# Kernel tuning notes

Measured on AMD Instinct MI355X. Metric: run time of the kernel, lower is better.

Reference implementation:

```python
import jax, jax.numpy as jnp
import numpy as np

XLIM = 10.0
N_BINS = 200
LATTICE = 12.42
N_O, N_H = 64, 128
T, R = 1000, 8


def setup_inputs() -> dict:
    key = jax.random.key(0)
    k1, k2 = jax.random.split(key)
    n = N_O + N_H
    stacked_radii = jax.random.uniform(k1, (T, R, n, 3), dtype=jnp.float32) * LATTICE
    lattices = jnp.full((3,), LATTICE, dtype=jnp.float32)
    gt_rdf = jax.random.uniform(k2, (3, N_BINS), dtype=jnp.float32)
    idx_O = jnp.arange(N_O, dtype=jnp.int32)
    idx_H = jnp.arange(N_H, dtype=jnp.int32) + N_O
    return {"stacked_radii": stacked_radii, "lattices": lattices,
            "gt_rdf": gt_rdf, "idx_O": idx_O, "idx_H": idx_H}


def reference(stacked_radii, lattices, gt_rdf, idx_O, idx_H):
    bins = jnp.linspace(1e-6, XLIM, N_BINS + 1, dtype=jnp.float32)
    # np.histogram normalization: rho * (4/3)pi (r_hi^3 - r_lo^3)
    shell = (4.0 / 3.0) * np.pi * (bins[1:] ** 3 - bins[:-1] ** 3)
    vol = jnp.prod(lattices)
    # wrap positions into the box (data_seq / L % 1 * L)
    x = stacked_radii / lattices % 1.0 * lattices
    x = jnp.transpose(x, (1, 0, 2, 3))  # [R, T, N, 3]

    def pair_rdf(x_rep, i0, i1):
        x0 = x_rep[:, i0]  # [T, n0, 3]
        x1 = x_rep[:, i1]  # [T, n1, 3]
        # all-pairs minimum-image distance under PBC
        delta = jnp.abs(x0[:, :, None, :] - x1[:, None, :, :])  # [T, n0, n1, 3]
        delta = jnp.where(delta > 0.5 * lattices, delta - lattices, delta)
        d = jnp.sqrt(jnp.sum(delta ** 2, axis=-1)).ravel()
        n_pairs = d.shape[0]  # includes zeros, matches original rho
        mask = (d != 0.0) & (d >= bins[0]) & (d <= bins[-1])
        bidx = jnp.clip(jnp.searchsorted(bins, d, side='right') - 1, 0, N_BINS - 1)
        hist = jax.ops.segment_sum(mask.astype(jnp.float32), bidx, num_segments=N_BINS)
        rho = n_pairs / vol
        return hist / (rho * shell)  # [N_BINS]

    pairs = [(idx_O, idx_O), (idx_H, idx_H), (idx_H, idx_O)]  # OO, HH, HO
    # sequential over replicas (like the original python loop) to bound memory
    rdfs = [jax.lax.map(lambda xr, i0=i0, i1=i1: pair_rdf(xr, i0, i1), x)
            for (i0, i1) in pairs]  # each [R, N_BINS]
    maes = jnp.stack([XLIM * jnp.mean(jnp.abs(r - g), axis=-1)
                      for r, g in zip(rdfs, gt_rdf)], axis=0)  # [3, R]
    max_maes = jnp.max(maes, axis=0)  # [R]
    rdf_stack = jnp.concatenate(rdfs, axis=-1)  # [R, 3*N_BINS]
    return rdf_stack, max_maes
```

## Files before the change

kernel.cpp:

```cpp
#include <hip/hip_runtime.h>
#include <math.h>

#define NUM_T   1000
#define NUM_R   8
#define NBINS   200
#define FPB     4
#define NCOPY   8
#define HSTR    601
#define TTSZ    224

__device__ __forceinline__ float approx_sqrt(float x) {
    float r; asm("v_sqrt_f32 %0, %1" : "=v"(r) : "v"(x)); return r;
}
__device__ __forceinline__ float fract_(float x) {
#if __has_builtin(__builtin_amdgcn_fractf)
    return __builtin_amdgcn_fractf(x);
#else
    return x - floorf(x);
#endif
}

__global__ __launch_bounds__(256) void rdf_hist_kernel(
    const float* __restrict__ radii,
    const float* __restrict__ lat,
    unsigned int* __restrict__ gh)
{
    #pragma clang fp contract(off)
    __shared__ float4 posOx[96], posH0[96], posH1[96];
    __shared__ float TT[TTSZ];
    __shared__ unsigned int hist[NCOPY * HSTR];

    const int tid = threadIdx.x;

    if (tid < TTSZ) {
        float v;
        if (tid <= 200) {
            float b;
            if (tid < NBINS) {
                const double step = (10.0 - 1e-6) / 200.0;
                b = (float)(1e-6 + (double)tid * step);
            } else {
                b = __uint_as_float(__float_as_uint(10.0f) + 1u);
            }
            unsigned lo = 0u, hi = 0x7F800000u;
            while (lo < hi) {
                unsigned mid = (lo + hi) >> 1;
                if (sqrtf(__uint_as_float(mid)) >= b) hi = mid; else lo = mid + 1;
            }
            v = __uint_as_float(lo);
        } else {
            v = __uint_as_float(0x7F800000u);
        }
        TT[tid] = v;
    }
    for (int i = tid; i < NCOPY * HSTR; i += 256) hist[i] = 0u;

    const float Lx = lat[0], Ly = lat[1], Lz = lat[2];
    __syncthreads();

    const float Tp = TT[200];
    const int   hc = ((tid >> 3) & (NCOPY - 1)) * HSTR;

#define PAIR(PI, PJ, HB, W)                                                  \
    {                                                                        \
        float tx = (PI).x - (PJ).x;                                          \
        float ty = (PI).y - (PJ).y;                                          \
        float tz = (PI).z - (PJ).z;                                          \
        float ax = fminf(fabsf(tx), Lx - fabsf(tx));                         \
        float ay = fminf(fabsf(ty), Ly - fabsf(ty));                         \
        float az = fminf(fabsf(tz), Lz - fabsf(tz));                         \
        float s  = (ax*ax + ay*ay) + az*az;                                  \
        float z  = approx_sqrt(s * 400.0f);                                  \
        int   k  = (int)z;                                                   \
        float m  = fract_(z);                                                \
        if (__builtin_expect(fabsf(m - 0.5f) > 0.49980f, 0)) {               \
            float tlo = TT[k], thi = TT[k + 1];                              \
            k += ((s >= thi) ? 1 : 0) - ((s < tlo) ? 1 : 0);                 \
            k = max(k, 0);                                                   \
        }                                                                    \
        if (s < Tp) atomicAdd(&hist[(HB) + k], (W));                         \
    }

    const int rep   = blockIdx.x & (NUM_R - 1);
    const int chunk = blockIdx.x / NUM_R;
    const int iO = tid & 63;
    const int q  = tid >> 6;
    const int hO = tid & 127;
    const int qh = tid >> 7;

    for (int f = 0; f < FPB; ++f) {
        const int t = chunk * FPB + f;
        const float* src = radii + ((size_t)t * NUM_R + rep) * (192 * 3);
        __syncthreads();
        if (tid < 192) {
            float vx = src[tid*3+0], vy = src[tid*3+1], vz = src[tid*3+2];
            float ux = vx / Lx; ux -= floorf(ux);
            float uy = vy / Ly; uy -= floorf(uy);
            float uz = vz / Lz; uz -= floorf(uz);
            float4 p = make_float4(ux*Lx, uy*Ly, uz*Lz, 0.0f);
            if (tid < 64)       { posOx[tid] = p;        if (tid < 32)  posOx[tid+64] = p; }
            else if (tid < 128) { int h = tid-64;  posH0[h] = p; if (h < 32) posH0[h+64] = p; }
            else                { int h = tid-128; posH1[h] = p; if (h < 32) posH1[h+64] = p; }
        }
        __syncthreads();

        {
            const float4 pi = posOx[iO];
            const int hb = hc + 0 * NBINS;
            const int jb = iO + q + 1;
            #pragma unroll
            for (int it = 0; it < 7; ++it) { float4 pj = posOx[jb + 4*it]; PAIR(pi, pj, hb, 2u); }
            if (q < 3 || iO < 32)          { float4 pj = posOx[jb + 28];   PAIR(pi, pj, hb, 2u); }
        }
        {
            const float4 pi = posH0[iO];
            const int hb = hc + 1 * NBINS;
            const int jb = iO + q + 1;
            #pragma unroll
            for (int it = 0; it < 7; ++it) { float4 pj = posH0[jb + 4*it]; PAIR(pi, pj, hb, 2u); }
            if (q < 3 || iO < 32)          { float4 pj = posH0[jb + 28];   PAIR(pi, pj, hb, 2u); }
        }
        {
            const float4 pi = posH1[iO];
            const int hb = hc + 1 * NBINS;
            const int jb = iO + q + 1;
            #pragma unroll
            for (int it = 0; it < 7; ++it) { float4 pj = posH1[jb + 4*it]; PAIR(pi, pj, hb, 2u); }
            if (q < 3 || iO < 32)          { float4 pj = posH1[jb + 28];   PAIR(pi, pj, hb, 2u); }
        }
        {
            const float4 pi = posH0[iO];
            const int hb = hc + 1 * NBINS;
            const int jb = q * 16;
            #pragma unroll
            for (int jj = 0; jj < 16; ++jj) { float4 pj = posH1[jb + jj]; PAIR(pi, pj, hb, 2u); }
        }
        {
            const float4 pi = (hO < 64) ? posH0[hO] : posH1[hO - 64];
            const int hb = hc + 2 * NBINS;
            const int jb = qh * 32;
            #pragma unroll
            for (int jj = 0; jj < 32; ++jj) { float4 pj = posOx[jb + jj]; PAIR(pi, pj, hb, 1u); }
        }
    }
#undef PAIR

    __syncthreads();
    for (int i = tid; i < 3 * NBINS; i += 256) {
        unsigned int v = 0;
        #pragma unroll
        for (int c = 0; c < NCOPY; ++c) v += hist[c * HSTR + i];
        if (v) atomicAdd(&gh[rep * 3 * NBINS + i], v);
    }
}

__global__ __launch_bounds__(256) void rdf_final_kernel(
    const unsigned int* __restrict__ gh,
    const float* __restrict__ gt,
    const float* __restrict__ lat,
    float* __restrict__ out)
{
    #pragma clang fp contract(off)
    const int rep = blockIdx.x;
    const int tid = threadIdx.x;
    __shared__ float bins[NBINS + 1];
    __shared__ float red[256];

    for (int i = tid; i <= NBINS; i += 256) {
        const double step = (10.0 - 1e-6) / 200.0;
        bins[i] = (i == NBINS) ? 10.0f : (float)(1e-6 + (double)i * step);
    }
    __syncthreads();

    const float vol = (lat[0] * lat[1]) * lat[2];
    const float C   = 4.18879020478639053f;
    const int npairs[3] = { NUM_T*64*64, NUM_T*128*128, NUM_T*128*64 };

    float maxmae = -3.0e38f;
    for (int p = 0; p < 3; ++p) {
        float diff = 0.0f;
        if (tid < NBINS) {
            float b0 = bins[tid], b1 = bins[tid + 1];
            float shell = C * (b1*b1*b1 - b0*b0*b0);
            float rho = (float)npairs[p] / vol;
            float g = (float)gh[(rep*3 + p)*NBINS + tid] / (rho * shell);
            out[rep*3*NBINS + p*NBINS + tid] = g;
            diff = fabsf(g - gt[p*NBINS + tid]);
        }
        red[tid] = diff;
        __syncthreads();
        for (int s = 128; s > 0; s >>= 1) {
            if (tid < s) red[tid] += red[tid + s];
            __syncthreads();
        }
        if (tid == 0) {
            float mae = 10.0f * (red[0] / 200.0f);
            if (mae > maxmae) maxmae = mae;
        }
        __syncthreads();
    }
    if (tid == 0) out[NUM_R*3*NBINS + rep] = maxmae;
}

extern "C" void kernel_launch(void* const* d_in, const int* in_sizes, int n_in,
                              void* d_out, int out_size, void* d_ws, size_t ws_size,
                              hipStream_t stream) {
    const float* radii = (const float*)d_in[0];
    const float* lat   = (const float*)d_in[1];
    const float* gt    = (const float*)d_in[2];
    unsigned int* gh   = (unsigned int*)d_ws;

    hipMemsetAsync(gh, 0, NUM_R * 3 * NBINS * sizeof(unsigned int), stream);

    dim3 grid(NUM_R * (NUM_T / FPB));
    hipLaunchKernelGGL(rdf_hist_kernel, grid, dim3(256), 0, stream,
                       radii, lat, gh);
    hipLaunchKernelGGL(rdf_final_kernel, dim3(NUM_R), dim3(256), 0, stream,
                       gh, gt, lat, (float*)d_out);
}
```

Measured before the change: 109.7 us.

## Prefetch next frame, branchless out-of-range atomics, wave-uniform ambiguity check, halve frames per block

Loads the next frame's raw positions into registers while the current frame's pairs are processed, so global latency overlaps compute. Replaces the per-lane range test with an unsigned-bit range compare that sends out-of-range pairs to a dummy bin (600) instead of predicating the atomic. It also makes the bin-boundary fixup branch wave-uniform via __any, and restructures the HO loop so each thread handles both H sets against shared O positions. FPB drops from 4 to 2, doubling the number of blocks. The cost is more LDS atomics on the dummy bin, which may contend, plus extra fixed setup per block.

Result: faster. 106.7 us (-2.7%).

```diff
diff --git a/kernel.cpp b/kernel.cpp
--- a/kernel.cpp
+++ b/kernel.cpp
@@ -4,7 +4,7 @@
 #define NUM_T   1000
 #define NUM_R   8
 #define NBINS   200
-#define FPB     4
+#define FPB     2
 #define NCOPY   8
 #define HSTR    601
 #define TTSZ    224
@@ -58,10 +58,11 @@
     const float Lx = lat[0], Ly = lat[1], Lz = lat[2];
     __syncthreads();
 
-    const float Tp = TT[200];
-    const int   hc = ((tid >> 3) & (NCOPY - 1)) * HSTR;
-
-#define PAIR(PI, PJ, HB, W)                                                  \
+    const unsigned T0b = __float_as_uint(TT[0]);
+    const unsigned Rng = __float_as_uint(TT[200]) - T0b;
+    const int      hc  = ((tid >> 3) & (NCOPY - 1)) * HSTR;
+
+#define PAIR(PI, PJ, TOFF, W)                                                \
     {                                                                        \
         float tx = (PI).x - (PJ).x;                                          \
         float ty = (PI).y - (PJ).y;                                          \
@@ -73,74 +74,73 @@
         float z  = approx_sqrt(s * 400.0f);                                  \
         int   k  = (int)z;                                                   \
         float m  = fract_(z);                                                \
-        if (__builtin_expect(fabsf(m - 0.5f) > 0.49980f, 0)) {               \
+        bool amb = fabsf(m - 0.5f) > 0.49980f;                               \
+        if (__builtin_expect(__any(amb), 0)) {                               \
             float tlo = TT[k], thi = TT[k + 1];                              \
             k += ((s >= thi) ? 1 : 0) - ((s < tlo) ? 1 : 0);                 \
-            k = max(k, 0);                                                   \
         }                                                                    \
-        if (s < Tp) atomicAdd(&hist[(HB) + k], (W));                         \
+        bool inr = (__float_as_uint(s) - T0b) < Rng;                         \
+        int  kk  = inr ? ((TOFF) + k) : 600;                                 \
+        atomicAdd(&hist[hc + kk], (W));                                      \
     }
 
     const int rep   = blockIdx.x & (NUM_R - 1);
     const int chunk = blockIdx.x / NUM_R;
-    const int iO = tid & 63;
-    const int q  = tid >> 6;
-    const int hO = tid & 127;
-    const int qh = tid >> 7;
-
+    const int l     = tid & 63;
+    const int q     = tid >> 6;
+
+    float rvx = 0.f, rvy = 0.f, rvz = 0.f;
+    {
+        const float* s0 = radii + ((size_t)(chunk * FPB) * NUM_R + rep) * (192 * 3);
+        if (tid < 192) { rvx = s0[tid*3+0]; rvy = s0[tid*3+1]; rvz = s0[tid*3+2]; }
+    }
+
+    #pragma unroll 1
     for (int f = 0; f < FPB; ++f) {
-        const int t = chunk * FPB + f;
-        const float* src = radii + ((size_t)t * NUM_R + rep) * (192 * 3);
         __syncthreads();
         if (tid < 192) {
-            float vx = src[tid*3+0], vy = src[tid*3+1], vz = src[tid*3+2];
-            float ux = vx / Lx; ux -= floorf(ux);
-            float uy = vy / Ly; uy -= floorf(uy);
-            float uz = vz / Lz; uz -= floorf(uz);
+            float ux = rvx / Lx; ux -= floorf(ux);
+            float uy = rvy / Ly; uy -= floorf(uy);
+            float uz = rvz / Lz; uz -= floorf(uz);
             float4 p = make_float4(ux*Lx, uy*Ly, uz*Lz, 0.0f);
-            if (tid < 64)       { posOx[tid] = p;        if (tid < 32)  posOx[tid+64] = p; }
+            if (tid < 64)       { posOx[tid] = p;  if (tid < 32) posOx[tid+64] = p; }
             else if (tid < 128) { int h = tid-64;  posH0[h] = p; if (h < 32) posH0[h+64] = p; }
             else                { int h = tid-128; posH1[h] = p; if (h < 32) posH1[h+64] = p; }
         }
         __syncthreads();
 
-        {
-            const float4 pi = posOx[iO];
-            const int hb = hc + 0 * NBINS;
-            const int jb = iO + q + 1;
-            #pragma unroll
-            for (int it = 0; it < 7; ++it) { float4 pj = posOx[jb + 4*it]; PAIR(pi, pj, hb, 2u); }
-            if (q < 3 || iO < 32)          { float4 pj = posOx[jb + 28];   PAIR(pi, pj, hb, 2u); }
-        }
-        {
-            const float4 pi = posH0[iO];
-            const int hb = hc + 1 * NBINS;
-            const int jb = iO + q + 1;
-            #pragma unroll
-            for (int it = 0; it < 7; ++it) { float4 pj = posH0[jb + 4*it]; PAIR(pi, pj, hb, 2u); }
-            if (q < 3 || iO < 32)          { float4 pj = posH0[jb + 28];   PAIR(pi, pj, hb, 2u); }
-        }
-        {
-            const float4 pi = posH1[iO];
-            const int hb = hc + 1 * NBINS;
-            const int jb = iO + q + 1;
-            #pragma unroll
-            for (int it = 0; it < 7; ++it) { float4 pj = posH1[jb + 4*it]; PAIR(pi, pj, hb, 2u); }
-            if (q < 3 || iO < 32)          { float4 pj = posH1[jb + 28];   PAIR(pi, pj, hb, 2u); }
-        }
-        {
-            const float4 pi = posH0[iO];
-            const int hb = hc + 1 * NBINS;
-            const int jb = q * 16;
-            #pragma unroll
-            for (int jj = 0; jj < 16; ++jj) { float4 pj = posH1[jb + jj]; PAIR(pi, pj, hb, 2u); }
-        }
-        {
-            const float4 pi = (hO < 64) ? posH0[hO] : posH1[hO - 64];
-            const int hb = hc + 2 * NBINS;
-            const int jb = qh * 32;
-            #pragma unroll
-            for (int jj = 0; jj < 32; ++jj) { float4 pj = posOx[jb + jj]; PAIR(pi, pj, hb, 1u); }
+        if (f + 1 < FPB && tid < 192) {
+            const float* s1 = radii + ((size_t)(chunk * FPB + f + 1) * NUM_R + rep) * (192 * 3);
+            rvx = s1[tid*3+0]; rvy = s1[tid*3+1]; rvz = s1[tid*3+2];
+        }
+
+        const float4 piO = posOx[l];
+        const float4 pi0 = posH0[l];
+        const float4 pi1 = posH1[l];
+        const int jb = l + q + 1;
+
+        #pragma unroll
+        for (int it = 0; it < 7; ++it) { float4 pj = posOx[jb + 4*it]; PAIR(piO, pj, 0, 2u); }
+        if (q < 3 || l < 32)           { float4 pj = posOx[jb + 28];   PAIR(piO, pj, 0, 2u); }
+
+        #pragma unroll
+        for (int it = 0; it < 7; ++it) { float4 pj = posH0[jb + 4*it]; PAIR(pi0, pj, 200, 2u); }
+        if (q < 3 || l < 32)           { float4 pj = posH0[jb + 28];   PAIR(pi0, pj, 200, 2u); }
+
+        #pragma unroll
+        for (int it = 0; it < 7; ++it) { float4 pj = posH1[jb + 4*it]; PAIR(pi1, pj, 200, 2u); }
+        if (q < 3 || l < 32)           { float4 pj = posH1[jb + 28];   PAIR(pi1, pj, 200, 2u); }
+
+        #pragma unroll 4
+        for (int jj = 0; jj < 16; ++jj) {
+            float4 pj = posH1[q * 16 + jj];
+            PAIR(pi0, pj, 200, 2u);
+        }
+        #pragma unroll 4
+        for (int jj = 0; jj < 16; ++jj) {
+            float4 pj = posOx[q * 16 + jj];
+            PAIR(pi0, pj, 400, 1u);
+            PAIR(pi1, pj, 400, 1u);
         }
     }
 #undef PAIR
```
